# Performance work log

Hardware: AMD Instinct MI355X
Metric: run time of the kernel (lower is better)

## Reference

```python
import jax, jax.numpy as jnp
import numpy as np

B, T, H, HY, E, L = 32, 256, 1024, 256, 64, 2


def setup_inputs() -> dict:
    key = jax.random.key(0)
    ks = jax.random.split(key, 16)
    rn = lambda k, s, sc=0.05: jax.random.normal(k, s, dtype=jnp.float32) * sc
    return {
        'input': rn(ks[0], (B, T, H), 1.0),
        'w_ih': rn(ks[1], (L, 4 * H, H)),
        'w_hh': rn(ks[2], (L, 4 * H, H)),
        'hyper_w_ih': rn(ks[3], (L, 4 * HY, 2 * H)),
        'hyper_w_hh': rn(ks[4], (L, 4 * HY, HY)),
        'hyper_b': rn(ks[5], (L, 4 * HY)),
        'w_zh': rn(ks[6], (L, 4 * E, HY)),
        'b_zh': jnp.ones((L, 4 * E), jnp.float32),
        'w_zx': rn(ks[7], (L, 4 * E, HY)),
        'b_zx': jnp.ones((L, 4 * E), jnp.float32),
        'w_zb': rn(ks[8], (L, 4 * E, HY)),
        'w_dh': rn(ks[9], (L, 4, H, E), 1.0 / E),
        'w_dx': rn(ks[10], (L, 4, H, E), 1.0 / E),
        'w_db': rn(ks[11], (L, 4, H, E)),
        'b0': rn(ks[12], (L, 4 * H)),
    }


def reference(input, w_ih, w_hh, hyper_w_ih, hyper_w_hh, hyper_b,
              w_zh, b_zh, w_zx, b_zx, w_zb, w_dh, w_dx, w_db, b0):
    L = w_ih.shape[0]
    Bb = input.shape[0]
    Hh = w_hh.shape[-1]
    Hy = hyper_w_hh.shape[-1]
    Ee = w_dh.shape[-1]

    def cell(l, xt, h, c, hh, hc):
        # hyper (meta) LSTM step: input is concat(x, h_main)
        xh = jnp.concatenate([xt, h], axis=-1)
        hg = xh @ hyper_w_ih[l].T + hh @ hyper_w_hh[l].T + hyper_b[l]
        hi, hf, hgc, ho = jnp.split(hg, 4, axis=-1)
        hc2 = jax.nn.sigmoid(hf) * hc + jax.nn.sigmoid(hi) * jnp.tanh(hgc)
        hh2 = jax.nn.sigmoid(ho) * jnp.tanh(hc2)
        # gate-wise embeddings z (B, 4, E) then project to per-gate scale vectors (B, 4H)
        zh = (hh2 @ w_zh[l].T + b_zh[l]).reshape(Bb, 4, Ee)
        zx = (hh2 @ w_zx[l].T + b_zx[l]).reshape(Bb, 4, Ee)
        zb = (hh2 @ w_zb[l].T).reshape(Bb, 4, Ee)
        dh = jnp.einsum('bge,ghe->bgh', zh, w_dh[l]).reshape(Bb, 4 * Hh)
        dx = jnp.einsum('bge,ghe->bgh', zx, w_dx[l]).reshape(Bb, 4 * Hh)
        db = jnp.einsum('bge,ghe->bgh', zb, w_db[l]).reshape(Bb, 4 * Hh) + b0[l]
        # main LSTM gates, dynamically scaled by hypernetwork
        pre = dh * (h @ w_hh[l].T) + dx * (xt @ w_ih[l].T) + db
        i, f, g, o = jnp.split(pre, 4, axis=-1)
        c2 = jax.nn.sigmoid(f) * c + jax.nn.sigmoid(i) * jnp.tanh(g)
        h2 = jax.nn.sigmoid(o) * jnp.tanh(c2)
        return h2, c2, hh2, hc2

    def step(carry, xt):
        h, c, hh, hc = carry  # each (L, B, .)
        hs, cs, hhs, hcs = [], [], [], []
        inp = xt
        for l in range(L):
            h2, c2, hh2, hc2 = cell(l, inp, h[l], c[l], hh[l], hc[l])
            inp = h2
            hs.append(h2); cs.append(c2); hhs.append(hh2); hcs.append(hc2)
        carry = (jnp.stack(hs), jnp.stack(cs), jnp.stack(hhs), jnp.stack(hcs))
        return carry, inp  # top-layer hidden

    init = (jnp.zeros((L, Bb, Hh), input.dtype), jnp.zeros((L, Bb, Hh), input.dtype),
            jnp.zeros((L, Bb, Hy), input.dtype), jnp.zeros((L, Bb, Hy), input.dtype))
    carry, ys = jax.lax.scan(step, init, jnp.swapaxes(input, 0, 1))
    h_seq = jnp.swapaxes(ys, 0, 1)  # (B, T, H)
    return h_seq, carry[0][-1], carry[1][-1]
```

## Files before the change

### kernel.cpp

```cpp
#include <hip/hip_runtime.h>

typedef __bf16 bf16;
typedef __bf16 bf16x8 __attribute__((ext_vector_type(8)));
typedef __bf16 bf16x4 __attribute__((ext_vector_type(4)));
typedef float f32x4 __attribute__((ext_vector_type(4)));
typedef unsigned long long u64;

#define SCOPE_AGENT __HIP_MEMORY_SCOPE_AGENT


__device__ __forceinline__ float sigf(float x) { return 1.0f / (1.0f + __expf(-x)); }
__device__ __forceinline__ float tanhf_fast(float x) {
  float e = __expf(-2.0f * fabsf(x));
  float r = (1.0f - e) / (1.0f + e);
  return copysignf(r, x);
}
__device__ __forceinline__ f32x4 mfma16(bf16x8 a, bf16x8 b, f32x4 c) {
  return __builtin_amdgcn_mfma_f32_16x16x32_bf16(a, b, c, 0, 0, 0);
}
__device__ __forceinline__ u64 uld(const u64* p) { return __hip_atomic_load(p, __ATOMIC_RELAXED, SCOPE_AGENT); }
__device__ __forceinline__ void ust(u64* p, u64 v) { __hip_atomic_store(p, v, __ATOMIC_RELAXED, SCOPE_AGENT); }
__device__ __forceinline__ int ildi(const int* p) { return __hip_atomic_load(p, __ATOMIC_RELAXED, SCOPE_AGENT); }
__device__ __forceinline__ void isti(int* p, int v) { __hip_atomic_store(p, v, __ATOMIC_RELAXED, SCOPE_AGENT); }
__device__ __forceinline__ void fstf(float* p, float v) { __hip_atomic_store(p, v, __ATOMIC_RELAXED, SCOPE_AGENT); }

__global__ void detect_kernel(const void* probe, int* flag) {
  __shared__ int cnt;
  if (threadIdx.x == 0) cnt = 0;
  __syncthreads();
  const bf16* p = (const bf16*)probe;
  int local = 0;
  for (int j = threadIdx.x; j < 8192; j += 256) {
    float x = (float)p[j];
    bool wild = (x != x) || (fabsf(x) > 1e3f) || (x != 0.0f && fabsf(x) < 1e-30f);
    local += wild ? 1 : 0;
  }
  atomicAdd(&cnt, local);
  __syncthreads();
  if (threadIdx.x == 0) *flag = (cnt > 64) ? 1 : 0;
}

struct CvtSrc { const void* s[15]; };
struct CvtDst { bf16* d[15]; };

__global__ __launch_bounds__(256) void convert_kernel(CvtSrc S, CvtDst D, const int* flag) {
  const int pre[16] = {0, 8388608, 16777216, 25165824, 29360128, 29884416, 29886464,
                       30017536, 30018048, 30149120, 30149632, 30280704, 30804992,
                       31329280, 31853568, 31861760};
  const int fp32 = *flag;
  const int nvec = 31861760 / 4;
  for (int v = blockIdx.x * 256 + threadIdx.x; v < nvec; v += gridDim.x * 256) {
    int e = v * 4;
    int seg = 0;
#pragma unroll
    for (int k = 1; k < 15; ++k) seg += (e >= pre[k]) ? 1 : 0;
    int off = e - pre[seg];
    bf16* d = D.d[seg] + off;
    if (fp32) {
      const float* s = (const float*)S.s[seg] + off;
      float4 x = *(const float4*)s;
      d[0] = (bf16)x.x; d[1] = (bf16)x.y; d[2] = (bf16)x.z; d[3] = (bf16)x.w;
    } else {
      const bf16* s = (const bf16*)S.s[seg] + off;
      d[0] = s[0]; d[1] = s[1]; d[2] = s[2]; d[3] = s[3];
    }
  }
}

__global__ void init_kernel(u64* zbase) {
  int i = blockIdx.x * 256 + threadIdx.x;
  zbase[i] = 0ull;
}

__global__ __launch_bounds__(256) void gemm_pre(
    const bf16* __restrict__ A, const bf16* __restrict__ w_ih_l,
    const bf16* __restrict__ hwih_l, bf16* __restrict__ Xp, float* __restrict__ Hxp) {
  constexpr int LDT = 72;
  __shared__ alignas(16) bf16 As[64 * LDT];
  __shared__ alignas(16) bf16 Bs[64 * LDT];
  const int bm = blockIdx.x & 127;
  const int bn = blockIdx.x >> 7;
  const int m0 = bm * 64, n0 = bn * 64;
  const int tid = threadIdx.x;
  const int lane = tid & 63, wid = tid >> 6;
  const int l15 = lane & 15, q = lane >> 4;
  const int srow = tid >> 2, sk = (tid & 3) * 16;
  const bf16* arow = A + (size_t)(m0 + srow) * 1024;
  const int n = n0 + srow;
  const bf16* brow = (n < 4096) ? (w_ih_l + (size_t)n * 1024)
                                : (hwih_l + (size_t)(n - 4096) * 2048);
  f32x4 acc[4] = {};
  for (int kb = 0; kb < 1024; kb += 64) {
    *(bf16x8*)(&As[srow * LDT + sk])     = *(const bf16x8*)(arow + kb + sk);
    *(bf16x8*)(&As[srow * LDT + sk + 8]) = *(const bf16x8*)(arow + kb + sk + 8);
    *(bf16x8*)(&Bs[srow * LDT + sk])     = *(const bf16x8*)(brow + kb + sk);
    *(bf16x8*)(&Bs[srow * LDT + sk + 8]) = *(const bf16x8*)(brow + kb + sk + 8);
    __syncthreads();
#pragma unroll
    for (int kk = 0; kk < 64; kk += 32) {
      bf16x8 av = *(const bf16x8*)(&As[(wid * 16 + l15) * LDT + kk + q * 8]);
#pragma unroll
      for (int j = 0; j < 4; ++j) {
        bf16x8 bv = *(const bf16x8*)(&Bs[(j * 16 + l15) * LDT + kk + q * 8]);
        acc[j] = mfma16(av, bv, acc[j]);
      }
    }
    __syncthreads();
  }
#pragma unroll
  for (int j = 0; j < 4; ++j) {
    const int gn = n0 + j * 16 + l15;
#pragma unroll
    for (int r = 0; r < 4; ++r) {
      const int gm = m0 + wid * 16 + q * 4 + r;
      float v = acc[j][r];
      if (gn < 4096) Xp[(size_t)gm * 4096 + gn] = (bf16)v;
      else           Hxp[(size_t)gm * 1024 + (gn - 4096)] = v;
    }
  }
}

struct SeqArgs {
  const bf16 *w_ih, *w_hh, *hwih, *hwhh, *hyb;
  const bf16 *w_zh, *b_zh, *w_zx, *b_zx, *w_zb;
  const bf16 *w_dh, *w_dx, *w_db, *b0;
  const bf16 *Xp; const float *Hxp;
  u64 *hpub, *hhpub, *x0pub; float *hgpub;
  float *outp;
  int *flags;
};

__global__ __launch_bounds__(256) void seq_kernel(SeqArgs a) {
  __shared__ char smem[60160] __attribute__((aligned(16)));
  bf16 (*hstage)[520]  = (bf16(*)[520])smem;
  bf16 (*hhstage)[264] = (bf16(*)[264])(smem + 33280);
  bf16 (*hA4)[1032]   = (bf16(*)[1032])smem;
  bf16 (*x0A4)[1032]  = (bf16(*)[1032])(smem + 8256);
  bf16 (*hh2A)[264]   = (bf16(*)[264])(smem + 16512);
  float (*RhL)[256]   = (float(*)[256])(smem + 18624);
  float (*XhL)[256]   = (float(*)[256])(smem + 22720);
  float (*hgs)[1024]  = (float(*)[1024])(smem + 26816);
  float (*zsL)[768]   = (float(*)[768])(smem + 43200);
  float (*presL)[256] = (float(*)[256])(smem + 55488);
  bf16 (*hbuf)[64]    = (bf16(*)[64])(smem + 59584);

  const int tid = threadIdx.x;
  const int lane = tid & 63, wid = tid >> 6;
  const int l15 = lane & 15, q = lane >> 4;
  const int blk = blockIdx.x;
  const int layer = blk >> 7;
  const int lblk = blk & 127;
  const int bq = lblk >> 4, s16 = lblk & 15;
  const bool isHyper = ((s16 >> 1) == bq);
  const int hj = bq * 2 + (s16 & 1);

  u64*   hpub  = a.hpub  + layer * 8192;
  u64*   hhpub = a.hhpub + layer * 2048;
  float* hgpub = a.hgpub + layer * 32768;
  int* genp  = a.flags + layer * 16;
  int* ogenp = a.flags + (1 - layer) * 16;
  int* arrp  = a.flags + 64 + layer * 2048;
  int* hgfp  = a.flags + 4160 + layer * 256;

  const bf16* whh_l = a.w_hh + (size_t)layer * 4194304;
  const bf16* hybl  = a.hyb + layer * 1024;
  const bf16* bzh_l = a.b_zh + layer * 256;
  const bf16* bzx_l = a.b_zx + layer * 256;
  const bf16* b0_l  = a.b0 + (size_t)layer * 4096;
  const int cb = tid >> 6, chl = tid & 63;

  float c_reg = 0.0f;
  float hc[4] = {0,0,0,0};

  const bf16* zrow[12];
#pragma unroll
  for (int j = 0; j < 12; ++j) {
    int ng = wid * 12 + j, tau = ng >> 4;
    const bf16* base = (tau == 0) ? a.w_zh : (tau == 1) ? a.w_zx : a.w_zb;
    zrow[j] = base + ((size_t)layer * 256 + (ng & 15) * 16 + l15) * 256;
  }
  const bf16* rrow[4];
  const bf16* xrow[4];
#pragma unroll
  for (int nt = 0; nt < 4; ++nt) {
    rrow[nt] = whh_l + (size_t)(wid * 1024 + s16 * 64 + nt * 16 + l15) * 1024;
    xrow[nt] = a.w_ih + (size_t)layer * 4194304
             + (size_t)(wid * 1024 + s16 * 64 + nt * 16 + l15) * 1024;
  }
  const size_t wdo = ((size_t)(layer * 4 + wid) * 1024 + s16 * 64 + lane) * 64;
  const bf16 *pdh = a.w_dh + wdo, *pdx = a.w_dx + wdo, *pdb = a.w_db + wdo;

  for (int t = 0; t < 256; ++t) {
    u64* x0slot = a.x0pub + (size_t)(t & 1) * 8192;
    if (t > 0 && tid == 0) {
      while (ildi(genp) < t) __builtin_amdgcn_s_sleep(2);
    }
    if (tid == 64) {
      const int need = layer ? (t + 1) : (t - 1);
      while (ildi(ogenp) < need) __builtin_amdgcn_s_sleep(2);
    }
    __atomic_signal_fence(__ATOMIC_SEQ_CST);
    __syncthreads();

    if (isHyper) {
      for (int i = tid; i < 2048; i += 256) {
        int b = i >> 6, u = i & 63;
        *(u64*)&hhstage[b][u * 4] = uld(hhpub + i);
      }
      const bf16* bihrow = a.hwih + (size_t)layer * 2097152
                         + (size_t)(hj * 64 + wid * 16 + l15) * 2048;
      f32x4 cA = {}, cB = {};
      for (int ph = layer ? 0 : 2; ph < 4; ++ph) {
        const u64* src = ((ph < 2) ? (const u64*)x0slot : (const u64*)hpub)
                       + ((ph & 1) << 7);
        for (int i = tid; i < 4096; i += 256) {
          int b = i >> 7, u = i & 127;
          *(u64*)&hstage[b][u * 4] = uld(src + ((size_t)b << 8) + u);
        }
        __syncthreads();
        const bf16* bw = bihrow + ph * 512;
        for (int kk = 0; kk < 512; kk += 32) {
          int ko = kk + q * 8;
          bf16x8 bv = *(const bf16x8*)(bw + ko);
          bf16x8 a0 = *(const bf16x8*)&hstage[l15][ko];
          bf16x8 a1 = *(const bf16x8*)&hstage[16 + l15][ko];
          cA = mfma16(a0, bv, cA); cB = mfma16(a1, bv, cB);
        }
        __syncthreads();
      }
      const bf16* bhh = a.hwhh + (size_t)layer * 262144
                      + (size_t)(hj * 64 + wid * 16 + l15) * 256;
      for (int kk = 0; kk < 256; kk += 32) {
        int ko = kk + q * 8;
        bf16x8 bv = *(const bf16x8*)(bhh + ko);
        bf16x8 a0 = *(const bf16x8*)&hhstage[l15][ko];
        bf16x8 a1 = *(const bf16x8*)&hhstage[16 + l15][ko];
        cA = mfma16(a0, bv, cA); cB = mfma16(a1, bv, cB);
      }
      const int n = hj * 64 + wid * 16 + l15;
#pragma unroll
      for (int r = 0; r < 4; ++r) {
        fstf(hgpub + (q * 4 + r) * 1024 + n, cA[r]);
        fstf(hgpub + (16 + q * 4 + r) * 1024 + n, cB[r]);
      }
      __atomic_signal_fence(__ATOMIC_SEQ_CST);
      __builtin_amdgcn_s_waitcnt(0);
      __syncthreads();
      if (tid == 0) isti(hgfp + hj * 16, t + 1);
    }
    __syncthreads();

    for (int i = tid; i < 1024; i += 256) {
      int b = i >> 8, u = i & 255;
      *(u64*)&hA4[b][u * 4] = uld(hpub + ((size_t)(bq * 4 + b) << 8) + u);
    }
    if (layer) {
      for (int i = tid; i < 1024; i += 256) {
        int b = i >> 8, u = i & 255;
        *(u64*)&x0A4[b][u * 4] = uld((const u64*)x0slot + ((size_t)(bq * 4 + b) << 8) + u);
      }
    }
    __syncthreads();
    {
      f32x4 racc[4] = {};
      f32x4 xacc[4] = {};
      for (int kk = 0; kk < 1024; kk += 32) {
        const int ko = kk + q * 8;
        bf16x8 av = *(const bf16x8*)&hA4[l15 & 3][ko];
#pragma unroll
        for (int nt = 0; nt < 4; ++nt) {
          bf16x8 bv = *(const bf16x8*)(rrow[nt] + ko);
          racc[nt] = mfma16(av, bv, racc[nt]);
        }
        if (layer) {
          bf16x8 axv = *(const bf16x8*)&x0A4[l15 & 3][ko];
#pragma unroll
          for (int nt = 0; nt < 4; ++nt) {
            bf16x8 bv = *(const bf16x8*)(xrow[nt] + ko);
            xacc[nt] = mfma16(axv, bv, xacc[nt]);
          }
        }
      }
      if (lane < 16) {
#pragma unroll
        for (int nt = 0; nt < 4; ++nt)
#pragma unroll
          for (int r = 0; r < 4; ++r) {
            RhL[r][wid * 64 + nt * 16 + lane] = racc[nt][r];
            if (layer) XhL[r][wid * 64 + nt * 16 + lane] = xacc[nt][r];
          }
      }
    }
    if (tid < 16) { while (ildi(hgfp + tid * 16) < t + 1) __builtin_amdgcn_s_sleep(1); }
    __atomic_signal_fence(__ATOMIC_SEQ_CST);
    __syncthreads();
    {
      const u64* hg64 = (const u64*)hgpub;
      for (int i = tid; i < 2048; i += 256) {
        int b = i >> 9, u = i & 511;
        *(u64*)&hgs[b][u * 2] = uld(hg64 + ((size_t)(bq * 4 + b) << 9) + u);
      }
    }
    __syncthreads();
    {
      const float* hgr = hgs[cb];
      const float* hxr = a.Hxp + ((size_t)(bq * 4 + cb) * 256 + t) * 1024;
      const int d0 = chl * 4;
      float hh2v[4];
#pragma unroll
      for (int dd = 0; dd < 4; ++dd) {
        int d = d0 + dd;
        float hi  = hgr[d]       + (float)hybl[d];
        float hf  = hgr[256 + d] + (float)hybl[256 + d];
        float hgv = hgr[512 + d] + (float)hybl[512 + d];
        float ho  = hgr[768 + d] + (float)hybl[768 + d];
        if (layer == 0) {
          hi += hxr[d]; hf += hxr[256 + d]; hgv += hxr[512 + d]; ho += hxr[768 + d];
        }
        hc[dd] = sigf(hf) * hc[dd] + sigf(hi) * tanhf_fast(hgv);
        float v = sigf(ho) * tanhf_fast(hc[dd]);
        hh2v[dd] = v;
        hh2A[cb][d] = (bf16)v;
      }
      if (s16 == 0) {
        union { bf16 h[4]; u64 v; } pk;
#pragma unroll
        for (int dd = 0; dd < 4; ++dd) pk.h[dd] = (bf16)hh2v[dd];
        ust(hhpub + ((size_t)(bq * 4 + cb) << 6) + chl, pk.v);
      }
    }
    __syncthreads();
    {
      f32x4 zacc[12] = {};
      for (int kk = 0; kk < 256; kk += 32) {
        const int ko = kk + q * 8;
        bf16x8 av = *(const bf16x8*)&hh2A[l15 & 3][ko];
#pragma unroll
        for (int j = 0; j < 12; ++j) {
          bf16x8 bv = *(const bf16x8*)(zrow[j] + ko);
          zacc[j] = mfma16(av, bv, zacc[j]);
        }
      }
      if (lane < 16) {
#pragma unroll
        for (int j = 0; j < 12; ++j) {
          int ng = wid * 12 + j, tau = ng >> 4, col = (ng & 15) * 16 + lane;
          float bias = (tau == 0) ? (float)bzh_l[col] : (tau == 1) ? (float)bzx_l[col] : 0.0f;
#pragma unroll
          for (int r = 0; r < 4; ++r) zsL[r][tau * 256 + col] = zacc[j][r] + bias;
        }
      }
    }
    __syncthreads();
    {
      float dH[4] = {}, dX[4] = {}, dB[4] = {};
      for (int e0 = 0; e0 < 64; e0 += 4) {
        bf16x4 wh = *(const bf16x4*)(pdh + e0);
        bf16x4 wx = *(const bf16x4*)(pdx + e0);
        bf16x4 wb = *(const bf16x4*)(pdb + e0);
        f32x4 zh_[4], zx_[4], zb_[4];
#pragma unroll
        for (int b = 0; b < 4; ++b) {
          zh_[b] = *(const f32x4*)&zsL[b][wid * 64 + e0];
          zx_[b] = *(const f32x4*)&zsL[b][256 + wid * 64 + e0];
          zb_[b] = *(const f32x4*)&zsL[b][512 + wid * 64 + e0];
        }
#pragma unroll
        for (int jj = 0; jj < 4; ++jj) {
          float whf = (float)wh[jj], wxf = (float)wx[jj], wbf = (float)wb[jj];
#pragma unroll
          for (int b = 0; b < 4; ++b) {
            dH[b] += zh_[b][jj] * whf;
            dX[b] += zx_[b][jj] * wxf;
            dB[b] += zb_[b][jj] * wbf;
          }
        }
      }
#pragma unroll
      for (int b = 0; b < 4; ++b) {
        float rh = RhL[b][wid * 64 + lane];
        float xp = layer ? XhL[b][wid * 64 + lane]
                         : (float)a.Xp[((size_t)(bq * 4 + b) * 256 + t) * 4096
                                       + wid * 1024 + s16 * 64 + lane];
        float b0v = (float)b0_l[wid * 1024 + s16 * 64 + lane];
        presL[b][wid * 64 + lane] = dH[b] * rh + dX[b] * xp + dB[b] + b0v;
      }
    }
    __syncthreads();
    {
      float iv = presL[cb][chl];
      float fv = presL[cb][64 + chl];
      float gv = presL[cb][128 + chl];
      float ov = presL[cb][192 + chl];
      c_reg = sigf(fv) * c_reg + sigf(iv) * tanhf_fast(gv);
      float hn = sigf(ov) * tanhf_fast(c_reg);
      hbuf[cb][chl] = (bf16)hn;
      if (layer) {
        const size_t oo = ((size_t)(bq * 4 + cb) * 256 + t) * 1024 + s16 * 64 + chl;
        a.outp[oo] = hn;
        if (t == 255) {
          a.outp[8388608 + (bq * 4 + cb) * 1024 + s16 * 64 + chl] = hn;
          a.outp[8421376 + (bq * 4 + cb) * 1024 + s16 * 64 + chl] = c_reg;
        }
      }
    }
    __syncthreads();
    if (tid < 64) {
      int b = tid >> 4, u = tid & 15;
      u64 pk = *(const u64*)&hbuf[b][u * 4];
      ust(hpub + ((size_t)(bq * 4 + b) << 8) + s16 * 16 + u, pk);
      if (layer == 0)
        ust(x0slot + ((size_t)(bq * 4 + b) << 8) + s16 * 16 + u, pk);
    }
    __atomic_signal_fence(__ATOMIC_SEQ_CST);
    __builtin_amdgcn_s_waitcnt(0);
    __syncthreads();
    if (tid == 0) isti(arrp + lblk * 16, t + 1);
    if (lblk == 0 && wid == 0) {
      const int t1 = t + 1;
      for (;;) {
        int v0 = ildi(arrp + lane * 32);
        int v1 = ildi(arrp + lane * 32 + 16);
        if (__all((v0 >= t1) && (v1 >= t1))) break;
        __builtin_amdgcn_s_sleep(2);
      }
      __atomic_signal_fence(__ATOMIC_SEQ_CST);
      if (lane == 0) isti(genp, t1);
    }
  }
}

extern "C" void kernel_launch(void* const* d_in, const int* in_sizes, int n_in,
                              void* d_out, int out_size, void* d_ws, size_t ws_size,
                              hipStream_t stream) {
  float* outp = (float*)d_out;
  char* ws = (char*)d_ws;
  bf16*  Xp     = (bf16*) (ws);
  float* Hxp    = (float*)(ws + 67108864ull);
  char*  pubb   = ws + 100663296ull;
  u64*   hpub   = (u64*)  (pubb + 0);
  u64*   hhpub  = (u64*)  (pubb + 131072);
  u64*   x0pub  = (u64*)  (pubb + 163840);
  int*   flags  = (int*)  (pubb + 294912);
  float* hgpub  = (float*)(pubb + 327680);
  bf16* c_input = (bf16*)(ws + 117669888ull);
  bf16* c_w_ih  = (bf16*)(ws + 134447104ull);
  bf16* c_w_hh  = (bf16*)(ws + 151224320ull);
  bf16* c_hwih  = (bf16*)(ws + 168001536ull);
  bf16* c_hwhh  = (bf16*)(ws + 176390144ull);
  bf16* c_hyb   = (bf16*)(ws + 177438720ull);
  bf16* c_wzh   = (bf16*)(ws + 177442816ull);
  bf16* c_bzh   = (bf16*)(ws + 177704960ull);
  bf16* c_wzx   = (bf16*)(ws + 177705984ull);
  bf16* c_bzx   = (bf16*)(ws + 177968128ull);
  bf16* c_wzb   = (bf16*)(ws + 177969152ull);
  bf16* c_wdh   = (bf16*)(ws + 178231296ull);
  bf16* c_wdx   = (bf16*)(ws + 179279872ull);
  bf16* c_wdb   = (bf16*)(ws + 180328448ull);
  bf16* c_b0    = (bf16*)(ws + 181377024ull);
  int*  dflag   = (int*) (ws + 181393408ull);

  hipLaunchKernelGGL(detect_kernel, dim3(1), dim3(256), 0, stream, d_in[2], dflag);
  CvtSrc S; CvtDst D;
  for (int i = 0; i < 15; ++i) S.s[i] = d_in[i];
  D.d[0] = c_input; D.d[1] = c_w_ih; D.d[2] = c_w_hh; D.d[3] = c_hwih; D.d[4] = c_hwhh;
  D.d[5] = c_hyb;   D.d[6] = c_wzh;  D.d[7] = c_bzh;  D.d[8] = c_wzx;  D.d[9] = c_bzx;
  D.d[10] = c_wzb;  D.d[11] = c_wdh; D.d[12] = c_wdx; D.d[13] = c_wdb; D.d[14] = c_b0;
  hipLaunchKernelGGL(convert_kernel, dim3(2048), dim3(256), 0, stream, S, D, dflag);

  hipLaunchKernelGGL(init_kernel, dim3(160), dim3(256), 0, stream, (u64*)pubb);
  hipLaunchKernelGGL(gemm_pre, dim3(10240), dim3(256), 0, stream,
                     c_input, c_w_ih, c_hwih, Xp, Hxp);

  SeqArgs sa;
  sa.w_ih = c_w_ih; sa.w_hh = c_w_hh; sa.hwih = c_hwih; sa.hwhh = c_hwhh; sa.hyb = c_hyb;
  sa.w_zh = c_wzh; sa.b_zh = c_bzh; sa.w_zx = c_wzx; sa.b_zx = c_bzx; sa.w_zb = c_wzb;
  sa.w_dh = c_wdh; sa.w_dx = c_wdx; sa.w_db = c_wdb; sa.b0 = c_b0;
  sa.Xp = Xp; sa.Hxp = Hxp;
  sa.hpub = hpub; sa.hhpub = hhpub; sa.x0pub = x0pub; sa.hgpub = hgpub;
  sa.outp = outp;
  sa.flags = flags;
  hipLaunchKernelGGL(seq_kernel, dim3(256), dim3(256), 0, stream, sa);
}
```

Before: 21.67 ms.

## Replace centralized generation barrier with distributed arrival polling and batch loads

```diff
diff --git a/kernel.cpp b/kernel.cpp
--- a/kernel.cpp
+++ b/kernel.cpp
@@ -157,9 +157,8 @@
   u64*   hpub  = a.hpub  + layer * 8192;
   u64*   hhpub = a.hhpub + layer * 2048;
   float* hgpub = a.hgpub + layer * 32768;
-  int* genp  = a.flags + layer * 16;
-  int* ogenp = a.flags + (1 - layer) * 16;
   int* arrp  = a.flags + 64 + layer * 2048;
+  int* oarrp = a.flags + 64 + (1 - layer) * 2048;
   int* hgfp  = a.flags + 4160 + layer * 256;
 
   const bf16* whh_l = a.w_hh + (size_t)layer * 4194304;
@@ -192,32 +191,71 @@
 
   for (int t = 0; t < 256; ++t) {
     u64* x0slot = a.x0pub + (size_t)(t & 1) * 8192;
-    if (t > 0 && tid == 0) {
-      while (ildi(genp) < t) __builtin_amdgcn_s_sleep(2);
-    }
-    if (tid == 64) {
+    if (t > 0 && tid < 64) {
+      for (;;) {
+        int v0 = ildi(arrp + lane * 32);
+        int v1 = ildi(arrp + lane * 32 + 16);
+        if (__all((v0 >= t) && (v1 >= t))) break;
+        __builtin_amdgcn_s_sleep(1);
+      }
+    }
+    if (tid >= 64 && tid < 128) {
       const int need = layer ? (t + 1) : (t - 1);
-      while (ildi(ogenp) < need) __builtin_amdgcn_s_sleep(2);
+      if (need > 0) {
+        for (;;) {
+          int v0 = ildi(oarrp + lane * 32);
+          int v1 = ildi(oarrp + lane * 32 + 16);
+          if (__all((v0 >= need) && (v1 >= need))) break;
+          __builtin_amdgcn_s_sleep(1);
+        }
+      }
     }
     __atomic_signal_fence(__ATOMIC_SEQ_CST);
     __syncthreads();
 
     if (isHyper) {
-      for (int i = tid; i < 2048; i += 256) {
-        int b = i >> 6, u = i & 63;
-        *(u64*)&hhstage[b][u * 4] = uld(hhpub + i);
+      {
+        u64 rhh[8];
+#pragma unroll
+        for (int k = 0; k < 8; ++k) rhh[k] = uld(hhpub + tid + k * 256);
+#pragma unroll
+        for (int k = 0; k < 8; ++k) {
+          int i = tid + k * 256;
+          *(u64*)&hhstage[i >> 6][(i & 63) * 4] = rhh[k];
+        }
       }
       const bf16* bihrow = a.hwih + (size_t)layer * 2097152
                          + (size_t)(hj * 64 + wid * 16 + l15) * 2048;
       f32x4 cA = {}, cB = {};
-      for (int ph = layer ? 0 : 2; ph < 4; ++ph) {
-        const u64* src = ((ph < 2) ? (const u64*)x0slot : (const u64*)hpub)
-                       + ((ph & 1) << 7);
-        for (int i = tid; i < 4096; i += 256) {
-          int b = i >> 7, u = i & 127;
-          *(u64*)&hstage[b][u * 4] = uld(src + ((size_t)b << 8) + u);
-        }
+      const int ph0 = layer ? 0 : 2;
+      u64 r16[16];
+      {
+        const u64* src = ((ph0 < 2) ? (const u64*)x0slot : (const u64*)hpub)
+                       + ((ph0 & 1) << 7);
+#pragma unroll
+        for (int k = 0; k < 16; ++k) {
+          int i = tid + k * 256;
+          r16[k] = uld(src + ((size_t)(i >> 7) << 8) + (i & 127));
+        }
+      }
+      for (int ph = ph0; ph < 4; ++ph) {
         __syncthreads();
+#pragma unroll
+        for (int k = 0; k < 16; ++k) {
+          int i = tid + k * 256;
+          *(u64*)&hstage[i >> 7][(i & 127) * 4] = r16[k];
+        }
+        __syncthreads();
+        if (ph < 3) {
+          const int pn = ph + 1;
+          const u64* src = ((pn < 2) ? (const u64*)x0slot : (const u64*)hpub)
+                         + ((pn & 1) << 7);
+#pragma unroll
+          for (int k = 0; k < 16; ++k) {
+            int i = tid + k * 256;
+            r16[k] = uld(src + ((size_t)(i >> 7) << 8) + (i & 127));
+          }
+        }
         const bf16* bw = bihrow + ph * 512;
         for (int kk = 0; kk < 512; kk += 32) {
           int ko = kk + q * 8;
@@ -226,7 +264,6 @@
           bf16x8 a1 = *(const bf16x8*)&hstage[16 + l15][ko];
           cA = mfma16(a0, bv, cA); cB = mfma16(a1, bv, cB);
         }
-        __syncthreads();
       }
       const bf16* bhh = a.hwhh + (size_t)layer * 262144
                       + (size_t)(hj * 64 + wid * 16 + l15) * 256;
@@ -250,14 +287,26 @@
     }
     __syncthreads();
 
-    for (int i = tid; i < 1024; i += 256) {
-      int b = i >> 8, u = i & 255;
-      *(u64*)&hA4[b][u * 4] = uld(hpub + ((size_t)(bq * 4 + b) << 8) + u);
-    }
-    if (layer) {
-      for (int i = tid; i < 1024; i += 256) {
-        int b = i >> 8, u = i & 255;
-        *(u64*)&x0A4[b][u * 4] = uld((const u64*)x0slot + ((size_t)(bq * 4 + b) << 8) + u);
+    {
+      u64 ra[4];
+#pragma unroll
+      for (int k = 0; k < 4; ++k)
+        ra[k] = uld(hpub + ((size_t)bq << 10) + tid + k * 256);
+      if (layer) {
+        u64 rx[4];
+#pragma unroll
+        for (int k = 0; k < 4; ++k)
+          rx[k] = uld((const u64*)x0slot + ((size_t)bq << 10) + tid + k * 256);
+#pragma unroll
+        for (int k = 0; k < 4; ++k) {
+          int i = tid + k * 256;
+          *(u64*)&x0A4[i >> 8][(i & 255) * 4] = rx[k];
+        }
+      }
+#pragma unroll
+      for (int k = 0; k < 4; ++k) {
+        int i = tid + k * 256;
+        *(u64*)&hA4[i >> 8][(i & 255) * 4] = ra[k];
       }
     }
     __syncthreads();
@@ -295,10 +344,14 @@
     __atomic_signal_fence(__ATOMIC_SEQ_CST);
     __syncthreads();
     {
-      const u64* hg64 = (const u64*)hgpub;
-      for (int i = tid; i < 2048; i += 256) {
-        int b = i >> 9, u = i & 511;
-        *(u64*)&hgs[b][u * 2] = uld(hg64 + ((size_t)(bq * 4 + b) << 9) + u);
+      const u64* hg64 = (const u64*)hgpub + ((size_t)bq << 11);
+      u64 rg[8];
+#pragma unroll
+      for (int k = 0; k < 8; ++k) rg[k] = uld(hg64 + tid + k * 256);
+#pragma unroll
+      for (int k = 0; k < 8; ++k) {
+        int i = tid + k * 256;
+        *(u64*)&hgs[i >> 9][(i & 511) * 2] = rg[k];
       }
     }
     __syncthreads();
@@ -416,17 +469,6 @@
     __builtin_amdgcn_s_waitcnt(0);
     __syncthreads();
     if (tid == 0) isti(arrp + lblk * 16, t + 1);
-    if (lblk == 0 && wid == 0) {
-      const int t1 = t + 1;
-      for (;;) {
-        int v0 = ildi(arrp + lane * 32);
-        int v1 = ildi(arrp + lane * 32 + 16);
-        if (__all((v0 >= t1) && (v1 >= t1))) break;
-        __builtin_amdgcn_s_sleep(2);
-      }
-      __atomic_signal_fence(__ATOMIC_SEQ_CST);
-      if (lane == 0) isti(genp, t1);
-    }
   }
 }
 
```

New measurement: 23.52 ms. +8.5%, slower.

## Batch layer-1 input projections into chunked GEMMs over stored layer-0 outputs

Applied to the files above, without the earlier changes.

```diff
diff --git a/kernel.cpp b/kernel.cpp
--- a/kernel.cpp
+++ b/kernel.cpp
@@ -121,11 +121,14 @@
 }
 
 struct SeqArgs {
-  const bf16 *w_ih, *w_hh, *hwih, *hwhh, *hyb;
+  const bf16 *w_hh, *hwih, *hwhh, *hyb;
   const bf16 *w_zh, *b_zh, *w_zx, *b_zx, *w_zb;
   const bf16 *w_dh, *w_dx, *w_db, *b0;
   const bf16 *Xp; const float *Hxp;
-  u64 *hpub, *hhpub, *x0pub; float *hgpub;
+  const bf16 *w_ih1;
+  bf16 *Xp1c; float *Hxp1c;
+  u64 *Y0;
+  u64 *hpub, *hhpub; float *hgpub;
   float *outp;
   int *flags;
 };
@@ -135,32 +138,37 @@
   bf16 (*hstage)[520]  = (bf16(*)[520])smem;
   bf16 (*hhstage)[264] = (bf16(*)[264])(smem + 33280);
   bf16 (*hA4)[1032]   = (bf16(*)[1032])smem;
-  bf16 (*x0A4)[1032]  = (bf16(*)[1032])(smem + 8256);
   bf16 (*hh2A)[264]   = (bf16(*)[264])(smem + 16512);
   float (*RhL)[256]   = (float(*)[256])(smem + 18624);
-  float (*XhL)[256]   = (float(*)[256])(smem + 22720);
   float (*hgs)[1024]  = (float(*)[1024])(smem + 26816);
   float (*zsL)[768]   = (float(*)[768])(smem + 43200);
   float (*presL)[256] = (float(*)[256])(smem + 55488);
   bf16 (*hbuf)[64]    = (bf16(*)[64])(smem + 59584);
+  bf16*  As = (bf16*)smem;
+  bf16*  Bs = (bf16*)(smem + 9216);
+  float* Ct = (float*)(smem + 18432);
 
   const int tid = threadIdx.x;
   const int lane = tid & 63, wid = tid >> 6;
   const int l15 = lane & 15, q = lane >> 4;
   const int blk = blockIdx.x;
-  const int layer = blk >> 7;
-  const int lblk = blk & 127;
-  const int bq = lblk >> 4, s16 = lblk & 15;
+  const int xcd = blk & 7, slot = blk >> 3;
+  const int layer = xcd >> 2, xl = xcd & 3;
+  const int s16 = xl * 4 + (slot & 3);
+  const int bq = slot >> 2;
+  const int lblk = bq * 16 + s16;
   const bool isHyper = ((s16 >> 1) == bq);
   const int hj = bq * 2 + (s16 & 1);
 
   u64*   hpub  = a.hpub  + layer * 8192;
   u64*   hhpub = a.hhpub + layer * 2048;
   float* hgpub = a.hgpub + layer * 32768;
-  int* genp  = a.flags + layer * 16;
-  int* ogenp = a.flags + (1 - layer) * 16;
-  int* arrp  = a.flags + 64 + layer * 2048;
-  int* hgfp  = a.flags + 4160 + layer * 256;
+  int* genp0  = a.flags;
+  int* genp   = a.flags + layer * 16;
+  int* gchunkp= a.flags + 32;
+  int* arrp   = a.flags + 64 + layer * 2048;
+  int* hgfp   = a.flags + 4160 + layer * 256;
+  int* carrp  = a.flags + 4672;
 
   const bf16* whh_l = a.w_hh + (size_t)layer * 4194304;
   const bf16* hybl  = a.hyb + layer * 1024;
@@ -180,24 +188,98 @@
     zrow[j] = base + ((size_t)layer * 256 + (ng & 15) * 16 + l15) * 256;
   }
   const bf16* rrow[4];
-  const bf16* xrow[4];
-#pragma unroll
-  for (int nt = 0; nt < 4; ++nt) {
+#pragma unroll
+  for (int nt = 0; nt < 4; ++nt)
     rrow[nt] = whh_l + (size_t)(wid * 1024 + s16 * 64 + nt * 16 + l15) * 1024;
-    xrow[nt] = a.w_ih + (size_t)layer * 4194304
-             + (size_t)(wid * 1024 + s16 * 64 + nt * 16 + l15) * 1024;
-  }
   const size_t wdo = ((size_t)(layer * 4 + wid) * 1024 + s16 * 64 + lane) * 64;
   const bf16 *pdh = a.w_dh + wdo, *pdx = a.w_dx + wdo, *pdb = a.w_db + wdo;
 
   for (int t = 0; t < 256; ++t) {
-    u64* x0slot = a.x0pub + (size_t)(t & 1) * 8192;
+    const int tloc = t & 31;
+
+    if (layer == 1 && tloc == 0) {
+      const int k = t >> 5;
+      if (tid == 0) { while (ildi(genp0) < (k + 1) * 32) __builtin_amdgcn_s_sleep(2); }
+      __atomic_signal_fence(__ATOMIC_SEQ_CST);
+      __syncthreads();
+      const int srow = tid >> 2, sk = (tid & 3) * 16;
+      for (int tt = 0; tt < 10; ++tt) {
+        const int tile = lblk * 10 + tt;
+        const int m0 = (tile & 15) * 64, n0 = (tile >> 4) * 64;
+        const int m = m0 + srow;
+        const u64* arow = a.Y0 + (((size_t)(m >> 5) * 256 + k * 32 + (m & 31)) << 8);
+        const int n = n0 + srow;
+        const bf16* brow = (n < 4096) ? (a.w_ih1 + (size_t)n * 1024)
+                                      : (a.hwih + 2097152 + (size_t)(n - 4096) * 2048);
+        f32x4 acc[4] = {};
+        for (int kb = 0; kb < 1024; kb += 64) {
+          const int c0 = (kb + sk) >> 2;
+          u64 a0 = uld(arow + c0),     a1 = uld(arow + c0 + 1);
+          u64 a2 = uld(arow + c0 + 2), a3 = uld(arow + c0 + 3);
+          *(u64*)&As[srow * 72 + sk]      = a0;
+          *(u64*)&As[srow * 72 + sk + 4]  = a1;
+          *(u64*)&As[srow * 72 + sk + 8]  = a2;
+          *(u64*)&As[srow * 72 + sk + 12] = a3;
+          *(bf16x8*)&Bs[srow * 72 + sk]     = *(const bf16x8*)(brow + kb + sk);
+          *(bf16x8*)&Bs[srow * 72 + sk + 8] = *(const bf16x8*)(brow + kb + sk + 8);
+          __syncthreads();
+#pragma unroll
+          for (int kk = 0; kk < 64; kk += 32) {
+            bf16x8 av = *(const bf16x8*)&As[(wid * 16 + l15) * 72 + kk + q * 8];
+#pragma unroll
+            for (int j = 0; j < 4; ++j) {
+              bf16x8 bv = *(const bf16x8*)&Bs[(j * 16 + l15) * 72 + kk + q * 8];
+              acc[j] = mfma16(av, bv, acc[j]);
+            }
+          }
+          __syncthreads();
+        }
+#pragma unroll
+        for (int j = 0; j < 4; ++j)
+#pragma unroll
+          for (int r = 0; r < 4; ++r)
+            Ct[(wid * 16 + q * 4 + r) * 64 + j * 16 + l15] = acc[j][r];
+        __syncthreads();
+#pragma unroll
+        for (int e = 0; e < 4; ++e) {
+          const int qd = tid * 4 + e;
+          const int row = qd >> 4, col4 = (qd & 15) * 4;
+          f32x4 v = *(const f32x4*)&Ct[row * 64 + col4];
+          const int gm = m0 + row, gn = n0 + col4;
+          if (gn < 4096) {
+            union { bf16 h[4]; u64 u; } pk;
+#pragma unroll
+            for (int x = 0; x < 4; ++x) pk.h[x] = (bf16)v[x];
+            ust((u64*)a.Xp1c + ((((size_t)gm << 12) + gn) >> 2), pk.u);
+          } else {
+            float* hp = a.Hxp1c + ((size_t)gm << 10) + (gn - 4096);
+#pragma unroll
+            for (int x = 0; x < 4; ++x) fstf(hp + x, v[x]);
+          }
+        }
+        __syncthreads();
+      }
+      __atomic_signal_fence(__ATOMIC_SEQ_CST);
+      __builtin_amdgcn_s_waitcnt(0);
+      __syncthreads();
+      if (tid == 0) isti(carrp + lblk * 16, k + 1);
+      if (lblk == 0 && wid == 0) {
+        for (;;) {
+          int v0 = ildi(carrp + lane * 32);
+          int v1 = ildi(carrp + lane * 32 + 16);
+          if (__all((v0 >= k + 1) && (v1 >= k + 1))) break;
+          __builtin_amdgcn_s_sleep(2);
+        }
+        __atomic_signal_fence(__ATOMIC_SEQ_CST);
+        if (lane == 0) isti(gchunkp, k + 1);
+      }
+      if (tid == 0) { while (ildi(gchunkp) < k + 1) __builtin_amdgcn_s_sleep(2); }
+      __atomic_signal_fence(__ATOMIC_SEQ_CST);
+      __syncthreads();
+    }
+
     if (t > 0 && tid == 0) {
       while (ildi(genp) < t) __builtin_amdgcn_s_sleep(2);
-    }
-    if (tid == 64) {
-      const int need = layer ? (t + 1) : (t - 1);
-      while (ildi(ogenp) < need) __builtin_amdgcn_s_sleep(2);
     }
     __atomic_signal_fence(__ATOMIC_SEQ_CST);
     __syncthreads();
@@ -207,26 +289,33 @@
         int b = i >> 6, u = i & 63;
         *(u64*)&hhstage[b][u * 4] = uld(hhpub + i);
       }
-      const bf16* bihrow = a.hwih + (size_t)layer * 2097152
-                         + (size_t)(hj * 64 + wid * 16 + l15) * 2048;
+      for (int i = tid; i < 4096; i += 256) {
+        int b = i >> 7, u = i & 127;
+        *(u64*)&hstage[b][u * 4] = uld(hpub + ((size_t)b << 8) + u);
+      }
+      __syncthreads();
+      const bf16* bih = a.hwih + (size_t)layer * 2097152
+                        + (size_t)(hj * 64 + wid * 16 + l15) * 2048 + 1024;
       f32x4 cA = {}, cB = {};
-      for (int ph = layer ? 0 : 2; ph < 4; ++ph) {
-        const u64* src = ((ph < 2) ? (const u64*)x0slot : (const u64*)hpub)
-                       + ((ph & 1) << 7);
-        for (int i = tid; i < 4096; i += 256) {
-          int b = i >> 7, u = i & 127;
-          *(u64*)&hstage[b][u * 4] = uld(src + ((size_t)b << 8) + u);
-        }
-        __syncthreads();
-        const bf16* bw = bihrow + ph * 512;
-        for (int kk = 0; kk < 512; kk += 32) {
-          int ko = kk + q * 8;
-          bf16x8 bv = *(const bf16x8*)(bw + ko);
-          bf16x8 a0 = *(const bf16x8*)&hstage[l15][ko];
-          bf16x8 a1 = *(const bf16x8*)&hstage[16 + l15][ko];
-          cA = mfma16(a0, bv, cA); cB = mfma16(a1, bv, cB);
-        }
-        __syncthreads();
+      for (int kk = 0; kk < 512; kk += 32) {
+        int ko = kk + q * 8;
+        bf16x8 bv = *(const bf16x8*)(bih + ko);
+        bf16x8 a0 = *(const bf16x8*)&hstage[l15][ko];
+        bf16x8 a1 = *(const bf16x8*)&hstage[16 + l15][ko];
+        cA = mfma16(a0, bv, cA); cB = mfma16(a1, bv, cB);
+      }
+      __syncthreads();
+      for (int i = tid; i < 4096; i += 256) {
+        int b = i >> 7, u = i & 127;
+        *(u64*)&hstage[b][u * 4] = uld(hpub + ((size_t)b << 8) + 128 + u);
+      }
+      __syncthreads();
+      for (int kk = 0; kk < 512; kk += 32) {
+        int ko = kk + q * 8;
+        bf16x8 bv = *(const bf16x8*)(bih + 512 + ko);
+        bf16x8 a0 = *(const bf16x8*)&hstage[l15][ko];
+        bf16x8 a1 = *(const bf16x8*)&hstage[16 + l15][ko];
+        cA = mfma16(a0, bv, cA); cB = mfma16(a1, bv, cB);
       }
       const bf16* bhh = a.hwhh + (size_t)layer * 262144
                       + (size_t)(hj * 64 + wid * 16 + l15) * 256;
@@ -254,16 +343,9 @@
       int b = i >> 8, u = i & 255;
       *(u64*)&hA4[b][u * 4] = uld(hpub + ((size_t)(bq * 4 + b) << 8) + u);
     }
-    if (layer) {
-      for (int i = tid; i < 1024; i += 256) {
-        int b = i >> 8, u = i & 255;
-        *(u64*)&x0A4[b][u * 4] = uld((const u64*)x0slot + ((size_t)(bq * 4 + b) << 8) + u);
-      }
-    }
     __syncthreads();
     {
       f32x4 racc[4] = {};
-      f32x4 xacc[4] = {};
       for (int kk = 0; kk < 1024; kk += 32) {
         const int ko = kk + q * 8;
         bf16x8 av = *(const bf16x8*)&hA4[l15 & 3][ko];
@@ -272,51 +354,57 @@
           bf16x8 bv = *(const bf16x8*)(rrow[nt] + ko);
           racc[nt] = mfma16(av, bv, racc[nt]);
         }
-        if (layer) {
-          bf16x8 axv = *(const bf16x8*)&x0A4[l15 & 3][ko];
-#pragma unroll
-          for (int nt = 0; nt < 4; ++nt) {
-            bf16x8 bv = *(const bf16x8*)(xrow[nt] + ko);
-            xacc[nt] = mfma16(axv, bv, xacc[nt]);
-          }
-        }
       }
       if (lane < 16) {
 #pragma unroll
         for (int nt = 0; nt < 4; ++nt)
 #pragma unroll
-          for (int r = 0; r < 4; ++r) {
+          for (int r = 0; r < 4; ++r)
             RhL[r][wid * 64 + nt * 16 + lane] = racc[nt][r];
-            if (layer) XhL[r][wid * 64 + nt * 16 + lane] = xacc[nt][r];
-          }
       }
     }
     if (tid < 16) { while (ildi(hgfp + tid * 16) < t + 1) __builtin_amdgcn_s_sleep(1); }
     __atomic_signal_fence(__ATOMIC_SEQ_CST);
     __syncthreads();
     {
-      const u64* hg64 = (const u64*)hgpub;
+      const u64* hg64 = (const u64*)hgpub + ((size_t)bq << 11);
       for (int i = tid; i < 2048; i += 256) {
         int b = i >> 9, u = i & 511;
-        *(u64*)&hgs[b][u * 2] = uld(hg64 + ((size_t)(bq * 4 + b) << 9) + u);
+        *(u64*)&hgs[b][u * 2] = uld(hg64 + ((size_t)b << 9) + u);
       }
     }
     __syncthreads();
     {
       const float* hgr = hgs[cb];
-      const float* hxr = a.Hxp + ((size_t)(bq * 4 + cb) * 256 + t) * 1024;
       const int d0 = chl * 4;
+      float hxv[4][4];
+      if (layer == 0) {
+        const float* hxr = a.Hxp + ((size_t)(bq * 4 + cb) * 256 + t) * 1024;
+#pragma unroll
+        for (int g = 0; g < 4; ++g)
+#pragma unroll
+          for (int dd = 0; dd < 4; ++dd) hxv[g][dd] = hxr[g * 256 + d0 + dd];
+      } else {
+        const u64* hxr = (const u64*)a.Hxp1c
+                       + ((size_t)((bq * 4 + cb) * 32 + tloc) << 9);
+#pragma unroll
+        for (int g = 0; g < 4; ++g) {
+          u64 w0 = uld(hxr + g * 128 + chl * 2);
+          u64 w1 = uld(hxr + g * 128 + chl * 2 + 1);
+          hxv[g][0] = __uint_as_float((unsigned)(w0 & 0xffffffffu));
+          hxv[g][1] = __uint_as_float((unsigned)(w0 >> 32));
+          hxv[g][2] = __uint_as_float((unsigned)(w1 & 0xffffffffu));
+          hxv[g][3] = __uint_as_float((unsigned)(w1 >> 32));
+        }
+      }
       float hh2v[4];
 #pragma unroll
       for (int dd = 0; dd < 4; ++dd) {
         int d = d0 + dd;
-        float hi  = hgr[d]       + (float)hybl[d];
-        float hf  = hgr[256 + d] + (float)hybl[256 + d];
-        float hgv = hgr[512 + d] + (float)hybl[512 + d];
-        float ho  = hgr[768 + d] + (float)hybl[768 + d];
-        if (layer == 0) {
-          hi += hxr[d]; hf += hxr[256 + d]; hgv += hxr[512 + d]; ho += hxr[768 + d];
-        }
+        float hi  = hgr[d]       + (float)hybl[d]       + hxv[0][dd];
+        float hf  = hgr[256 + d] + (float)hybl[256 + d] + hxv[1][dd];
+        float hgv = hgr[512 + d] + (float)hybl[512 + d] + hxv[2][dd];
+        float ho  = hgr[768 + d] + (float)hybl[768 + d] + hxv[3][dd];
         hc[dd] = sigf(hf) * hc[dd] + sigf(hi) * tanhf_fast(hgv);
         float v = sigf(ho) * tanhf_fast(hc[dd]);
         hh2v[dd] = v;
@@ -376,13 +464,19 @@
           }
         }
       }
+      const int n = wid * 1024 + s16 * 64 + lane;
 #pragma unroll
       for (int b = 0; b < 4; ++b) {
         float rh = RhL[b][wid * 64 + lane];
-        float xp = layer ? XhL[b][wid * 64 + lane]
-                         : (float)a.Xp[((size_t)(bq * 4 + b) * 256 + t) * 4096
-                                       + wid * 1024 + s16 * 64 + lane];
-        float b0v = (float)b0_l[wid * 1024 + s16 * 64 + lane];
+        float xp;
+        if (layer == 0) {
+          xp = (float)a.Xp[((size_t)(bq * 4 + b) * 256 + t) * 4096 + n];
+        } else {
+          u64 w = uld((const u64*)a.Xp1c
+                      + ((((size_t)((bq * 4 + b) * 32 + tloc) << 12) + (n & ~3)) >> 2));
+          xp = __uint_as_float(((unsigned)(w >> ((n & 3) * 16)) & 0xffffu) << 16);
+        }
+        float b0v = (float)b0_l[n];
         presL[b][wid * 64 + lane] = dH[b] * rh + dX[b] * xp + dB[b] + b0v;
       }
     }
@@ -410,7 +504,7 @@
       u64 pk = *(const u64*)&hbuf[b][u * 4];
       ust(hpub + ((size_t)(bq * 4 + b) << 8) + s16 * 16 + u, pk);
       if (layer == 0)
-        ust(x0slot + ((size_t)(bq * 4 + b) << 8) + s16 * 16 + u, pk);
+        ust(a.Y0 + (((size_t)(bq * 4 + b) * 256 + t) << 8) + s16 * 16 + u, pk);
     }
     __atomic_signal_fence(__ATOMIC_SEQ_CST);
     __builtin_amdgcn_s_waitcnt(0);
@@ -437,13 +531,10 @@
   char* ws = (char*)d_ws;
   bf16*  Xp     = (bf16*) (ws);
   float* Hxp    = (float*)(ws + 67108864ull);
-  char*  pubb   = ws + 100663296ull;
-  u64*   hpub   = (u64*)  (pubb + 0);
-  u64*   hhpub  = (u64*)  (pubb + 131072);
-  u64*   x0pub  = (u64*)  (pubb + 163840);
-  int*   flags  = (int*)  (pubb + 294912);
-  float* hgpub  = (float*)(pubb + 327680);
+  u64*   Y0     = (u64*)  (ws + 100663296ull);
   bf16* c_input = (bf16*)(ws + 117669888ull);
+  bf16*  Xp1c   = c_input;
+  float* Hxp1c  = (float*)(ws + 117669888ull + 8388608ull);
   bf16* c_w_ih  = (bf16*)(ws + 134447104ull);
   bf16* c_w_hh  = (bf16*)(ws + 151224320ull);
   bf16* c_hwih  = (bf16*)(ws + 168001536ull);
@@ -459,6 +550,11 @@
   bf16* c_wdb   = (bf16*)(ws + 180328448ull);
   bf16* c_b0    = (bf16*)(ws + 181377024ull);
   int*  dflag   = (int*) (ws + 181393408ull);
+  char* pubb    = ws + 181397504ull;
+  u64*   hpub   = (u64*)  (pubb + 0);
+  u64*   hhpub  = (u64*)  (pubb + 131072);
+  float* hgpub  = (float*)(pubb + 163840);
+  int*   flags  = (int*)  (pubb + 425984);
 
   hipLaunchKernelGGL(detect_kernel, dim3(1), dim3(256), 0, stream, d_in[2], dflag);
   CvtSrc S; CvtDst D;
@@ -468,16 +564,19 @@
   D.d[10] = c_wzb;  D.d[11] = c_wdh; D.d[12] = c_wdx; D.d[13] = c_wdb; D.d[14] = c_b0;
   hipLaunchKernelGGL(convert_kernel, dim3(2048), dim3(256), 0, stream, S, D, dflag);
 
-  hipLaunchKernelGGL(init_kernel, dim3(160), dim3(256), 0, stream, (u64*)pubb);
+  hipLaunchKernelGGL(init_kernel, dim3(224), dim3(256), 0, stream, (u64*)pubb);
   hipLaunchKernelGGL(gemm_pre, dim3(10240), dim3(256), 0, stream,
                      c_input, c_w_ih, c_hwih, Xp, Hxp);
 
   SeqArgs sa;
-  sa.w_ih = c_w_ih; sa.w_hh = c_w_hh; sa.hwih = c_hwih; sa.hwhh = c_hwhh; sa.hyb = c_hyb;
+  sa.w_hh = c_w_hh; sa.hwih = c_hwih; sa.hwhh = c_hwhh; sa.hyb = c_hyb;
   sa.w_zh = c_wzh; sa.b_zh = c_bzh; sa.w_zx = c_wzx; sa.b_zx = c_bzx; sa.w_zb = c_wzb;
   sa.w_dh = c_wdh; sa.w_dx = c_wdx; sa.w_db = c_wdb; sa.b0 = c_b0;
   sa.Xp = Xp; sa.Hxp = Hxp;
-  sa.hpub = hpub; sa.hhpub = hhpub; sa.x0pub = x0pub; sa.hgpub = hgpub;
+  sa.w_ih1 = c_w_ih + (size_t)4194304;
+  sa.Xp1c = Xp1c; sa.Hxp1c = Hxp1c;
+  sa.Y0 = Y0;
+  sa.hpub = hpub; sa.hhpub = hhpub; sa.hgpub = hgpub;
   sa.outp = outp;
   sa.flags = flags;
   hipLaunchKernelGGL(seq_kernel, dim3(256), dim3(256), 0, stream, sa);
```

After: 22.79 ms. +5.2%, slower.
